# Performance work log

Measured on AMD Instinct MI355X. Metric: run time of the kernel, lower is better.

The kernel has to match this reference:

```python
import jax, jax.numpy as jnp
import numpy as np

P = 200000   # num POIs
U = 50000    # num users / hyperedges
NNZ = 2000000
D = 64       # emb_dim
NUM_LAYERS = 3
DROPOUT = 0.5
VAL_SCALE = 0.05  # keep stacked-layer magnitudes stable (acts like degree normalization)


def spmm(rows, cols, vals, x, n_rows):
    # COO sparse [n_rows, n_cols] @ dense [n_cols, d]
    gathered = vals[:, None] * x[cols]          # [nnz, d]
    return jax.ops.segment_sum(gathered, rows, num_segments=n_rows)


def setup_inputs() -> dict:
    key = jax.random.key(0)
    ks = jax.random.split(key, 7)
    pois_embs = jax.random.normal(ks[0], (P, D), dtype=jnp.float32)
    up_rows = jax.random.randint(ks[1], (NNZ,), 0, U)
    up_cols = jax.random.randint(ks[2], (NNZ,), 0, P)
    up_vals = jax.random.uniform(ks[3], (NNZ,), dtype=jnp.float32) * VAL_SCALE
    pu_rows = jax.random.randint(ks[4], (NNZ,), 0, P)
    pu_cols = jax.random.randint(ks[5], (NNZ,), 0, U)
    pu_vals = jax.random.uniform(ks[6], (NNZ,), dtype=jnp.float32) * VAL_SCALE
    return {"pois_embs": pois_embs,
            "up_rows": up_rows, "up_cols": up_cols, "up_vals": up_vals,
            "pu_rows": pu_rows, "pu_cols": pu_cols, "pu_vals": pu_vals}


def reference(pois_embs, up_rows, up_cols, up_vals, pu_rows, pu_cols, pu_vals):
    keep = 1.0 - DROPOUT
    dk = jax.random.key(42)
    x = pois_embs
    acc = pois_embs                      # running sum for the final mean
    for layer_idx in range(NUM_LAYERS):
        msg = spmm(up_rows, up_cols, up_vals, x, U)        # HG_up @ x    -> [U, D]
        prop = spmm(pu_rows, pu_cols, pu_vals, msg, P)     # HG_pu @ msg  -> [P, D]
        x = prop + x                                       # residual
        mask = jax.random.bernoulli(jax.random.fold_in(dk, layer_idx), keep, x.shape)
        x = jnp.where(mask, x / keep, 0.0)                 # dropout (training mode)
        acc = acc + x
    return acc / (NUM_LAYERS + 1)
```

## Files before the change

### kernel.cpp

```cpp
#include <hip/hip_runtime.h>
#include <stdint.h>


#define DIM 64
#define SCAN_BLOCK 256
#define SCAN_ITEMS 4
#define SCAN_CHUNK (SCAN_BLOCK * SCAN_ITEMS)

#define NB_PART 512
#define BSHIFT 10
#define BROWS (1 << BSHIFT)
#define NBUCKET_PAD 256

__host__ __device__ __forceinline__ uint32_t rotl32(uint32_t v, int d) {
    return (v << d) | (v >> (32 - d));
}

__host__ __device__ __forceinline__ void threefry2x32(uint32_t k0, uint32_t k1,
                                                      uint32_t& x0, uint32_t& x1) {
    const uint32_t ks0 = k0, ks1 = k1, ks2 = k0 ^ k1 ^ 0x1BD11BDAu;
    x0 += ks0; x1 += ks1;
    x0 += x1; x1 = rotl32(x1, 13); x1 ^= x0;
    x0 += x1; x1 = rotl32(x1, 15); x1 ^= x0;
    x0 += x1; x1 = rotl32(x1, 26); x1 ^= x0;
    x0 += x1; x1 = rotl32(x1, 6);  x1 ^= x0;
    x0 += ks1; x1 += ks2 + 1u;
    x0 += x1; x1 = rotl32(x1, 17); x1 ^= x0;
    x0 += x1; x1 = rotl32(x1, 29); x1 ^= x0;
    x0 += x1; x1 = rotl32(x1, 16); x1 ^= x0;
    x0 += x1; x1 = rotl32(x1, 24); x1 ^= x0;
    x0 += ks2; x1 += ks0 + 2u;
    x0 += x1; x1 = rotl32(x1, 13); x1 ^= x0;
    x0 += x1; x1 = rotl32(x1, 15); x1 ^= x0;
    x0 += x1; x1 = rotl32(x1, 26); x1 ^= x0;
    x0 += x1; x1 = rotl32(x1, 6);  x1 ^= x0;
    x0 += ks0; x1 += ks1 + 3u;
    x0 += x1; x1 = rotl32(x1, 17); x1 ^= x0;
    x0 += x1; x1 = rotl32(x1, 29); x1 ^= x0;
    x0 += x1; x1 = rotl32(x1, 16); x1 ^= x0;
    x0 += x1; x1 = rotl32(x1, 24); x1 ^= x0;
    x0 += ks1; x1 += ks2 + 4u;
    x0 += x1; x1 = rotl32(x1, 13); x1 ^= x0;
    x0 += x1; x1 = rotl32(x1, 15); x1 ^= x0;
    x0 += x1; x1 = rotl32(x1, 26); x1 ^= x0;
    x0 += x1; x1 = rotl32(x1, 6);  x1 ^= x0;
    x0 += ks2; x1 += ks0 + 5u;
}

__global__ void init_kernel(const float4* __restrict__ pois, float4* __restrict__ x,
                            float4* __restrict__ out, int n4) {
    int i = blockIdx.x * blockDim.x + threadIdx.x;
    if (i < n4) {
        float4 v = pois[i];
        x[i] = v;
        out[i] = make_float4(0.25f * v.x, 0.25f * v.y, 0.25f * v.z, 0.25f * v.w);
    }
}


__global__ void scan1_kernel(const int* __restrict__ cnt, int* __restrict__ start,
                             int* __restrict__ bsum, int n) {
    __shared__ int lds[SCAN_BLOCK];
    int base = blockIdx.x * SCAN_CHUNK + threadIdx.x * SCAN_ITEMS;
    int v[SCAN_ITEMS];
    int s = 0;
#pragma unroll
    for (int i = 0; i < SCAN_ITEMS; ++i) {
        int idx = base + i;
        v[i] = (idx < n) ? cnt[idx] : 0;
        s += v[i];
    }
    lds[threadIdx.x] = s;
    __syncthreads();
    for (int off = 1; off < SCAN_BLOCK; off <<= 1) {
        int t = (threadIdx.x >= off) ? lds[threadIdx.x - off] : 0;
        __syncthreads();
        lds[threadIdx.x] += t;
        __syncthreads();
    }
    if (threadIdx.x == SCAN_BLOCK - 1) bsum[blockIdx.x] = lds[SCAN_BLOCK - 1];
    int run = (threadIdx.x == 0) ? 0 : lds[threadIdx.x - 1];
#pragma unroll
    for (int i = 0; i < SCAN_ITEMS; ++i) {
        int idx = base + i;
        if (idx < n) start[idx] = run;
        run += v[i];
    }
}

__global__ void scan2_kernel(int* __restrict__ bsum, int nb) {
    __shared__ int lds[SCAN_BLOCK];
    int v = (threadIdx.x < nb) ? bsum[threadIdx.x] : 0;
    lds[threadIdx.x] = v;
    __syncthreads();
    for (int off = 1; off < SCAN_BLOCK; off <<= 1) {
        int t = (threadIdx.x >= off) ? lds[threadIdx.x - off] : 0;
        __syncthreads();
        lds[threadIdx.x] += t;
        __syncthreads();
    }
    int excl = (threadIdx.x == 0) ? 0 : lds[threadIdx.x - 1];
    if (threadIdx.x < nb) bsum[threadIdx.x] = excl;
}

__global__ void scan3_kernel(int* __restrict__ start, int* __restrict__ work,
                             const int* __restrict__ bsum, int n) {
    int off = bsum[blockIdx.x];
    int base = blockIdx.x * SCAN_CHUNK;
#pragma unroll
    for (int i = 0; i < SCAN_ITEMS; ++i) {
        int idx = base + i * SCAN_BLOCK + threadIdx.x;
        if (idx < n) {
            int s = start[idx] + off;
            start[idx] = s;
            work[idx] = s;
        }
    }
}

__global__ void partA_count(const int* __restrict__ up_rows, const int* __restrict__ pu_rows,
                            int* __restrict__ counts, int U, int nnz, int chunk) {
    __shared__ int h[NBUCKET_PAD];
    int blk = blockIdx.x;
    for (int t = threadIdx.x; t < NBUCKET_PAD; t += blockDim.x) h[t] = 0;
    __syncthreads();
    int s = blk * chunk, e = min(nnz, s + chunk);
    for (int i = s + (int)threadIdx.x; i < e; i += blockDim.x) {
        atomicAdd(&h[up_rows[i] >> BSHIFT], 1);
        atomicAdd(&h[(U + pu_rows[i]) >> BSHIFT], 1);
    }
    __syncthreads();
    for (int t = threadIdx.x; t < NBUCKET_PAD; t += blockDim.x)
        counts[t * NB_PART + blk] = h[t];
}

__global__ void partB_reorder(const int* __restrict__ up_rows, const int* __restrict__ up_cols,
                              const float* __restrict__ up_vals,
                              const int* __restrict__ pu_rows, const int* __restrict__ pu_cols,
                              const float* __restrict__ pu_vals,
                              const int* __restrict__ base, uint2* __restrict__ stage,
                              int U, int nnz, int chunk) {
    __shared__ int tick[NBUCKET_PAD];
    int blk = blockIdx.x;
    for (int t = threadIdx.x; t < NBUCKET_PAD; t += blockDim.x)
        tick[t] = base[t * NB_PART + blk];
    __syncthreads();
    int s = blk * chunk, e = min(nnz, s + chunk);
    for (int i = s + (int)threadIdx.x; i < e; i += blockDim.x) {
        int r0 = up_rows[i];
        unsigned c0 = (unsigned)up_cols[i];
        float v0 = up_vals[i];
        int p0 = atomicAdd(&tick[r0 >> BSHIFT], 1);
        stage[p0] = make_uint2(((unsigned)(r0 & (BROWS - 1)) << 18) | c0,
                               __float_as_uint(v0));
        int r1 = U + pu_rows[i];
        unsigned c1 = (unsigned)pu_cols[i];
        float v1 = pu_vals[i];
        int p1 = atomicAdd(&tick[r1 >> BSHIFT], 1);
        stage[p1] = make_uint2(((unsigned)(r1 & (BROWS - 1)) << 18) | c1,
                               __float_as_uint(v1));
    }
}

__global__ void partC_finalize(const uint2* __restrict__ stage, const int* __restrict__ base,
                               uint2* __restrict__ pair, int* __restrict__ start,
                               int* __restrict__ cnt, int M) {
    __shared__ int h[BROWS];
    __shared__ int part[256];
    int b = blockIdx.x;
    int rowbase = b << BSHIFT;
    int bs = base[b * NB_PART];
    int be = base[(b + 1) * NB_PART];
    int t = threadIdx.x;
    for (int i = t; i < BROWS; i += 256) h[i] = 0;
    __syncthreads();
    for (int i = bs + t; i < be; i += 256)
        atomicAdd(&h[stage[i].x >> 18], 1);
    __syncthreads();
    int v0 = h[4 * t], v1 = h[4 * t + 1], v2 = h[4 * t + 2], v3 = h[4 * t + 3];
    part[t] = v0 + v1 + v2 + v3;
    __syncthreads();
    for (int off = 1; off < 256; off <<= 1) {
        int u = (t >= off) ? part[t - off] : 0;
        __syncthreads();
        part[t] += u;
        __syncthreads();
    }
    int run = bs + ((t == 0) ? 0 : part[t - 1]);
    int o0 = run, o1 = run + v0, o2 = o1 + v1, o3 = o2 + v2;
    int r0 = rowbase + 4 * t;
    if (r0     < M) { start[r0]     = o0; cnt[r0]     = v0; }
    if (r0 + 1 < M) { start[r0 + 1] = o1; cnt[r0 + 1] = v1; }
    if (r0 + 2 < M) { start[r0 + 2] = o2; cnt[r0 + 2] = v2; }
    if (r0 + 3 < M) { start[r0 + 3] = o3; cnt[r0 + 3] = v3; }
    __syncthreads();
    h[4 * t] = o0; h[4 * t + 1] = o1; h[4 * t + 2] = o2; h[4 * t + 3] = o3;
    __syncthreads();
    for (int i = bs + t; i < be; i += 256) {
        uint2 rec = stage[i];
        int pos = atomicAdd(&h[rec.x >> 18], 1);
        pair[pos] = make_uint2(rec.x & 0x3FFFFu, rec.y);
    }
}


__global__ void hist2_kernel(const int* __restrict__ up_rows, const int* __restrict__ pu_rows,
                             int* __restrict__ cnt, int U, int nnz) {
    int i = blockIdx.x * blockDim.x + threadIdx.x;
    if (i < nnz) {
        atomicAdd(&cnt[up_rows[i]], 1);
        atomicAdd(&cnt[U + pu_rows[i]], 1);
    }
}

__global__ void scatter2_kernel(const int* __restrict__ up_rows, const int* __restrict__ up_cols,
                                const float* __restrict__ up_vals,
                                const int* __restrict__ pu_rows, const int* __restrict__ pu_cols,
                                const float* __restrict__ pu_vals,
                                int* __restrict__ work, uint2* __restrict__ pair,
                                int U, int nnz) {
    int i = blockIdx.x * blockDim.x + threadIdx.x;
    if (i < nnz) {
        int pos0 = atomicAdd(&work[up_rows[i]], 1);
        pair[pos0] = make_uint2((unsigned)up_cols[i], __float_as_uint(up_vals[i]));
        int pos1 = atomicAdd(&work[U + pu_rows[i]], 1);
        pair[pos1] = make_uint2((unsigned)pu_cols[i], __float_as_uint(pu_vals[i]));
    }
}


__device__ __forceinline__ float4 shfl_xor_add4(float4 a, int mask) {
    a.x += __shfl_xor(a.x, mask, 64);
    a.y += __shfl_xor(a.y, mask, 64);
    a.z += __shfl_xor(a.z, mask, 64);
    a.w += __shfl_xor(a.w, mask, 64);
    return a;
}

__device__ __forceinline__ float4 row_accumulate(const uint2* __restrict__ pair,
                                                 const float4* __restrict__ src4,
                                                 int s, int c, int sub, int d4) {
    float4 acc = make_float4(0.f, 0.f, 0.f, 0.f);
    int j = sub;
    for (; j + 4 < c; j += 8) {
        uint2 p0 = pair[s + j];
        uint2 p1 = pair[s + j + 4];
        float4 g0 = src4[(size_t)p0.x * 16 + d4];
        float4 g1 = src4[(size_t)p1.x * 16 + d4];
        float v0 = __uint_as_float(p0.y);
        float v1 = __uint_as_float(p1.y);
        acc.x += v0 * g0.x + v1 * g1.x;
        acc.y += v0 * g0.y + v1 * g1.y;
        acc.z += v0 * g0.z + v1 * g1.z;
        acc.w += v0 * g0.w + v1 * g1.w;
    }
    if (j < c) {
        uint2 p0 = pair[s + j];
        float4 g0 = src4[(size_t)p0.x * 16 + d4];
        float v0 = __uint_as_float(p0.y);
        acc.x += v0 * g0.x;
        acc.y += v0 * g0.y;
        acc.z += v0 * g0.z;
        acc.w += v0 * g0.w;
    }
    acc = shfl_xor_add4(acc, 16);
    acc = shfl_xor_add4(acc, 32);
    return acc;
}

__global__ void spmm_gather(const int* __restrict__ start, const int* __restrict__ cnt,
                            const uint2* __restrict__ pair,
                            const float4* __restrict__ x4, float4* __restrict__ out4,
                            int nrows) {
    int wid = (blockIdx.x * blockDim.x + threadIdx.x) >> 6;
    int lane = threadIdx.x & 63;
    if (wid >= nrows) return;
    int sub = lane >> 4, d4 = lane & 15;
    float4 acc = row_accumulate(pair, x4, start[wid], cnt[wid], sub, d4);
    if (sub == 0) out4[(size_t)wid * 16 + d4] = acc;
}

__global__ void spmm_fused(const int* __restrict__ start, const int* __restrict__ cnt,
                           const uint2* __restrict__ pair,
                           const float4* __restrict__ msg4, float* __restrict__ x,
                           float* __restrict__ out, uint32_t k0, uint32_t k1, int nrows) {
    int wid = (blockIdx.x * blockDim.x + threadIdx.x) >> 6;
    int lane = threadIdx.x & 63;
    if (wid >= nrows) return;
    int sub = lane >> 4, d4 = lane & 15;
    float4 acc = row_accumulate(pair, msg4, start[wid], cnt[wid], sub, d4);
    int srcl = lane >> 2;
    float a0 = __shfl(acc.x, srcl, 64);
    float a1 = __shfl(acc.y, srcl, 64);
    float a2 = __shfl(acc.z, srcl, 64);
    float a3 = __shfl(acc.w, srcl, 64);
    int comp = lane & 3;
    float av = (comp & 2) ? ((comp & 1) ? a3 : a2) : ((comp & 1) ? a1 : a0);
    size_t idx = (size_t)wid * DIM + lane;
    float a = av + x[idx];
    uint32_t hi = 0u, lo = (uint32_t)idx;
    threefry2x32(k0, k1, hi, lo);
    float nx = ((hi ^ lo) & 0x80000000u) ? 0.0f : 2.0f * a;
    x[idx] = nx;
    out[idx] += 0.25f * nx;
}

extern "C" void kernel_launch(void* const* d_in, const int* in_sizes, int n_in,
                              void* d_out, int out_size, void* d_ws, size_t ws_size,
                              hipStream_t stream) {
    const float* pois    = (const float*)d_in[0];
    const int*   up_rows = (const int*)d_in[1];
    const int*   up_cols = (const int*)d_in[2];
    const float* up_vals = (const float*)d_in[3];
    const int*   pu_rows = (const int*)d_in[4];
    const int*   pu_cols = (const int*)d_in[5];
    const float* pu_vals = (const float*)d_in[6];
    float* out = (float*)d_out;

    const int n   = in_sizes[0];
    const int nnz = in_sizes[1];
    const int P   = n / DIM;
    const int U   = 50000;
    const int mU  = U * DIM;
    const int M   = U + P;
    const int NBUCKET = (M + BROWS - 1) >> BSHIFT;
    const int NT  = NBUCKET_PAD * NB_PART;
    const int total2 = 2 * nnz;

    float* x     = (float*)d_ws;
    float* msg   = x + n;
    int*   start = (int*)(msg + mU);
    int*   cnt   = start + M;
    int*   counts = cnt + M;
    int*   basea  = counts + NT;
    int*   bsum   = basea + NT;
    uint2* stage  = (uint2*)(bsum + 256);
    uint2* pair   = stage + total2;
    size_t needed = ((char*)(pair + total2)) - ((char*)d_ws);

    const int n4 = n / 4;
    init_kernel<<<(n4 + 255) / 256, 256, 0, stream>>>(
        (const float4*)pois, (float4*)x, (float4*)out, n4);

    if (needed <= ws_size) {
        const int chunk = (nnz + NB_PART - 1) / NB_PART;
        partA_count<<<NB_PART, 256, 0, stream>>>(up_rows, pu_rows, counts, U, nnz, chunk);
        int nb1 = (NT + SCAN_CHUNK - 1) / SCAN_CHUNK;
        scan1_kernel<<<nb1, SCAN_BLOCK, 0, stream>>>(counts, basea, bsum, NT);
        scan2_kernel<<<1, SCAN_BLOCK, 0, stream>>>(bsum, nb1);
        scan3_kernel<<<nb1, SCAN_BLOCK, 0, stream>>>(basea, basea, bsum, NT);
        partB_reorder<<<NB_PART, 256, 0, stream>>>(up_rows, up_cols, up_vals,
                                                   pu_rows, pu_cols, pu_vals,
                                                   basea, stage, U, nnz, chunk);
        partC_finalize<<<NBUCKET, 256, 0, stream>>>(stage, basea, pair, start, cnt, M);
    } else {
        int* work = counts;
        uint2* pairF = (uint2*)(((uintptr_t)(work + M) + 7) & ~(uintptr_t)7);
        pair = pairF;
        const int nzb = (nnz + 255) / 256;
        const int nbM = (M + SCAN_CHUNK - 1) / SCAN_CHUNK;
        hipMemsetAsync(cnt, 0, (size_t)M * sizeof(int), stream);
        hist2_kernel<<<nzb, 256, 0, stream>>>(up_rows, pu_rows, cnt, U, nnz);
        int* bsumF = (int*)(pairF + total2);
        scan1_kernel<<<nbM, SCAN_BLOCK, 0, stream>>>(cnt, start, bsumF, M);
        scan2_kernel<<<1, SCAN_BLOCK, 0, stream>>>(bsumF, nbM);
        scan3_kernel<<<nbM, SCAN_BLOCK, 0, stream>>>(start, work, bsumF, M);
        scatter2_kernel<<<nzb, 256, 0, stream>>>(up_rows, up_cols, up_vals,
                                                 pu_rows, pu_cols, pu_vals,
                                                 work, pair, U, nnz);
    }

    const long long thU = (long long)U * 64;
    const long long thP = (long long)P * 64;
    const int gU = (int)((thU + 255) / 256);
    const int gP = (int)((thP + 255) / 256);
    for (int l = 0; l < 3; ++l) {
        spmm_gather<<<gU, 256, 0, stream>>>(start, cnt, pair,
                                            (const float4*)x, (float4*)msg, U);
        uint32_t kk0 = 0u, kk1 = (uint32_t)l;
        threefry2x32(0u, 42u, kk0, kk1);
        spmm_fused<<<gP, 256, 0, stream>>>(start + U, cnt + U, pair,
                                           (const float4*)msg, x, out, kk0, kk1, P);
    }
}
```

Baseline: 800.0 us.

## Fold init copy into first layer and widen partC finalize blocks

Removes the init kernel that copied the POI embeddings into x and wrote a scaled copy to out. The first layer now reads pois directly, and a templated fused SpMM writes out from the residual input plus the new value. The last layer skips writing x back. Separately, the bucket-finalize kernel now runs with 512 threads, each handling two rows and two records per iteration, to raise parallelism in the CSR build. The cost is extra template instantiations and a longer scan in the finalize kernel.

```diff
diff --git a/kernel.cpp b/kernel.cpp
--- a/kernel.cpp
+++ b/kernel.cpp
@@ -11,6 +11,7 @@
 #define BSHIFT 10
 #define BROWS (1 << BSHIFT)
 #define NBUCKET_PAD 256
+#define CTHREADS 512
 
 __host__ __device__ __forceinline__ uint32_t rotl32(uint32_t v, int d) {
     return (v << d) | (v >> (32 - d));
@@ -47,16 +48,6 @@
     x0 += ks2; x1 += ks0 + 5u;
 }
 
-__global__ void init_kernel(const float4* __restrict__ pois, float4* __restrict__ x,
-                            float4* __restrict__ out, int n4) {
-    int i = blockIdx.x * blockDim.x + threadIdx.x;
-    if (i < n4) {
-        float4 v = pois[i];
-        x[i] = v;
-        out[i] = make_float4(0.25f * v.x, 0.25f * v.y, 0.25f * v.z, 0.25f * v.w);
-    }
-}
-
 
 __global__ void scan1_kernel(const int* __restrict__ cnt, int* __restrict__ start,
                              int* __restrict__ bsum, int n) {
@@ -166,40 +157,52 @@
                                uint2* __restrict__ pair, int* __restrict__ start,
                                int* __restrict__ cnt, int M) {
     __shared__ int h[BROWS];
-    __shared__ int part[256];
+    __shared__ int part[CTHREADS];
     int b = blockIdx.x;
     int rowbase = b << BSHIFT;
     int bs = base[b * NB_PART];
     int be = base[(b + 1) * NB_PART];
     int t = threadIdx.x;
-    for (int i = t; i < BROWS; i += 256) h[i] = 0;
-    __syncthreads();
-    for (int i = bs + t; i < be; i += 256)
-        atomicAdd(&h[stage[i].x >> 18], 1);
-    __syncthreads();
-    int v0 = h[4 * t], v1 = h[4 * t + 1], v2 = h[4 * t + 2], v3 = h[4 * t + 3];
-    part[t] = v0 + v1 + v2 + v3;
-    __syncthreads();
-    for (int off = 1; off < 256; off <<= 1) {
+    h[t] = 0;
+    h[t + CTHREADS] = 0;
+    __syncthreads();
+    for (int i = bs + t; i < be; i += 2 * CTHREADS) {
+        uint32_t a0 = stage[i].x;
+        int i1 = i + CTHREADS;
+        bool has1 = i1 < be;
+        uint32_t a1 = has1 ? stage[i1].x : 0u;
+        atomicAdd(&h[a0 >> 18], 1);
+        if (has1) atomicAdd(&h[a1 >> 18], 1);
+    }
+    __syncthreads();
+    int v0 = h[2 * t], v1 = h[2 * t + 1];
+    part[t] = v0 + v1;
+    __syncthreads();
+    for (int off = 1; off < CTHREADS; off <<= 1) {
         int u = (t >= off) ? part[t - off] : 0;
         __syncthreads();
         part[t] += u;
         __syncthreads();
     }
     int run = bs + ((t == 0) ? 0 : part[t - 1]);
-    int o0 = run, o1 = run + v0, o2 = o1 + v1, o3 = o2 + v2;
-    int r0 = rowbase + 4 * t;
+    int o0 = run, o1 = run + v0;
+    int r0 = rowbase + 2 * t;
     if (r0     < M) { start[r0]     = o0; cnt[r0]     = v0; }
     if (r0 + 1 < M) { start[r0 + 1] = o1; cnt[r0 + 1] = v1; }
-    if (r0 + 2 < M) { start[r0 + 2] = o2; cnt[r0 + 2] = v2; }
-    if (r0 + 3 < M) { start[r0 + 3] = o3; cnt[r0 + 3] = v3; }
-    __syncthreads();
-    h[4 * t] = o0; h[4 * t + 1] = o1; h[4 * t + 2] = o2; h[4 * t + 3] = o3;
-    __syncthreads();
-    for (int i = bs + t; i < be; i += 256) {
-        uint2 rec = stage[i];
-        int pos = atomicAdd(&h[rec.x >> 18], 1);
-        pair[pos] = make_uint2(rec.x & 0x3FFFFu, rec.y);
+    __syncthreads();
+    h[2 * t] = o0; h[2 * t + 1] = o1;
+    __syncthreads();
+    for (int i = bs + t; i < be; i += 2 * CTHREADS) {
+        uint2 rec0 = stage[i];
+        int i1 = i + CTHREADS;
+        bool has1 = i1 < be;
+        uint2 rec1 = has1 ? stage[i1] : make_uint2(0u, 0u);
+        int p0 = atomicAdd(&h[rec0.x >> 18], 1);
+        pair[p0] = make_uint2(rec0.x & 0x3FFFFu, rec0.y);
+        if (has1) {
+            int p1 = atomicAdd(&h[rec1.x >> 18], 1);
+            pair[p1] = make_uint2(rec1.x & 0x3FFFFu, rec1.y);
+        }
     }
 }
 
@@ -280,10 +283,12 @@
     if (sub == 0) out4[(size_t)wid * 16 + d4] = acc;
 }
 
-__global__ void spmm_fused(const int* __restrict__ start, const int* __restrict__ cnt,
-                           const uint2* __restrict__ pair,
-                           const float4* __restrict__ msg4, float* __restrict__ x,
-                           float* __restrict__ out, uint32_t k0, uint32_t k1, int nrows) {
+template <bool FIRST, bool LAST>
+__global__ void spmm_fused_t(const int* __restrict__ start, const int* __restrict__ cnt,
+                             const uint2* __restrict__ pair,
+                             const float4* __restrict__ msg4,
+                             const float* __restrict__ xres, float* __restrict__ xout,
+                             float* __restrict__ out, uint32_t k0, uint32_t k1, int nrows) {
     int wid = (blockIdx.x * blockDim.x + threadIdx.x) >> 6;
     int lane = threadIdx.x & 63;
     if (wid >= nrows) return;
@@ -297,12 +302,14 @@
     int comp = lane & 3;
     float av = (comp & 2) ? ((comp & 1) ? a3 : a2) : ((comp & 1) ? a1 : a0);
     size_t idx = (size_t)wid * DIM + lane;
-    float a = av + x[idx];
+    float xv = xres[idx];
+    float a = av + xv;
     uint32_t hi = 0u, lo = (uint32_t)idx;
     threefry2x32(k0, k1, hi, lo);
     float nx = ((hi ^ lo) & 0x80000000u) ? 0.0f : 2.0f * a;
-    x[idx] = nx;
-    out[idx] += 0.25f * nx;
+    if (!LAST) xout[idx] = nx;
+    if (FIRST) out[idx] = 0.25f * (xv + nx);
+    else       out[idx] += 0.25f * nx;
 }
 
 extern "C" void kernel_launch(void* const* d_in, const int* in_sizes, int n_in,
@@ -327,20 +334,16 @@
     const int NT  = NBUCKET_PAD * NB_PART;
     const int total2 = 2 * nnz;
 
-    float* x     = (float*)d_ws;
-    float* msg   = x + n;
-    int*   start = (int*)(msg + mU);
-    int*   cnt   = start + M;
+    float* x      = (float*)d_ws;
+    float* msg    = x + n;
+    int*   start  = (int*)(msg + mU);
+    int*   cnt    = start + M;
     int*   counts = cnt + M;
     int*   basea  = counts + NT;
     int*   bsum   = basea + NT;
     uint2* stage  = (uint2*)(bsum + 256);
     uint2* pair   = stage + total2;
     size_t needed = ((char*)(pair + total2)) - ((char*)d_ws);
-
-    const int n4 = n / 4;
-    init_kernel<<<(n4 + 255) / 256, 256, 0, stream>>>(
-        (const float4*)pois, (float4*)x, (float4*)out, n4);
 
     if (needed <= ws_size) {
         const int chunk = (nnz + NB_PART - 1) / NB_PART;
@@ -352,7 +355,7 @@
         partB_reorder<<<NB_PART, 256, 0, stream>>>(up_rows, up_cols, up_vals,
                                                    pu_rows, pu_cols, pu_vals,
                                                    basea, stage, U, nnz, chunk);
-        partC_finalize<<<NBUCKET, 256, 0, stream>>>(stage, basea, pair, start, cnt, M);
+        partC_finalize<<<NBUCKET, CTHREADS, 0, stream>>>(stage, basea, pair, start, cnt, M);
     } else {
         int* work = counts;
         uint2* pairF = (uint2*)(((uintptr_t)(work + M) + 7) & ~(uintptr_t)7);
@@ -374,12 +377,27 @@
     const long long thP = (long long)P * 64;
     const int gU = (int)((thU + 255) / 256);
     const int gP = (int)((thP + 255) / 256);
+
+    uint32_t key0[3], key1[3];
     for (int l = 0; l < 3; ++l) {
-        spmm_gather<<<gU, 256, 0, stream>>>(start, cnt, pair,
-                                            (const float4*)x, (float4*)msg, U);
         uint32_t kk0 = 0u, kk1 = (uint32_t)l;
         threefry2x32(0u, 42u, kk0, kk1);
-        spmm_fused<<<gP, 256, 0, stream>>>(start + U, cnt + U, pair,
-                                           (const float4*)msg, x, out, kk0, kk1, P);
-    }
-}
+        key0[l] = kk0; key1[l] = kk1;
+    }
+
+    spmm_gather<<<gU, 256, 0, stream>>>(start, cnt, pair,
+                                        (const float4*)pois, (float4*)msg, U);
+    spmm_fused_t<true, false><<<gP, 256, 0, stream>>>(start + U, cnt + U, pair,
+                                                      (const float4*)msg, pois, x,
+                                                      out, key0[0], key1[0], P);
+    spmm_gather<<<gU, 256, 0, stream>>>(start, cnt, pair,
+                                        (const float4*)x, (float4*)msg, U);
+    spmm_fused_t<false, false><<<gP, 256, 0, stream>>>(start + U, cnt + U, pair,
+                                                       (const float4*)msg, x, x,
+                                                       out, key0[1], key1[1], P);
+    spmm_gather<<<gU, 256, 0, stream>>>(start, cnt, pair,
+                                        (const float4*)x, (float4*)msg, U);
+    spmm_fused_t<false, true><<<gP, 256, 0, stream>>>(start + U, cnt + U, pair,
+                                                      (const float4*)msg, x, x,
+                                                      out, key0[2], key1[2], P);
+}
```

New measurement: 725.4 us. 9.3% less time.
